# Kernel optimization log

Hardware: AMD Instinct MI355X
Metric: run time of the kernel (lower is better)

Reference implementation:

```python
import jax, jax.numpy as jnp
import numpy as np

HEADS = 16
DIM_HEAD = 64
WINDOW = 128
LOOK_BACKWARD = 1
LOOK_FORWARD = 0
THETA = 10000.0
PAD_VALUE = -1


def look_around(x, backward, forward, pad_value, axis):
    """Gather overlapping windows: concat shifted copies along the intra-window axis."""
    w = x.shape[axis]
    size = backward + forward + 1
    pads = [(0, 0)] * x.ndim
    pads[axis] = (backward, forward)
    p = jnp.pad(x, pads, constant_values=pad_value)
    segs = [jax.lax.slice_in_dim(p, s, s + w, axis=axis) for s in range(size)]
    return jnp.concatenate(segs, axis=axis + 1)


def rotate_half(t):
    t1, t2 = jnp.split(t, 2, axis=-1)
    return jnp.concatenate([-t2, t1], axis=-1)


def setup_inputs() -> dict:
    key = jax.random.key(0)
    k1, k2, k3 = jax.random.split(key, 3)
    dim = 1024
    x = jax.random.normal(k1, (4, 4096, dim), dtype=jnp.float32)
    W_qkv = jax.random.normal(k2, (dim, 3 * HEADS * DIM_HEAD), dtype=jnp.float32) * (dim ** -0.5)
    W_out = jax.random.normal(k3, (HEADS * DIM_HEAD, dim), dtype=jnp.float32) * ((HEADS * DIM_HEAD) ** -0.5)
    return {"x": x, "W_qkv": W_qkv, "W_out": W_out}


def reference(x, W_qkv, W_out):
    b, n, dim = x.shape
    h, dh, ws = HEADS, DIM_HEAD, WINDOW
    w = n // ws
    j = ws * (LOOK_BACKWARD + LOOK_FORWARD + 1)  # 256 keys per query window

    qkv = x @ W_qkv  # (b, n, 3*h*dh)
    q, k, v = jnp.split(qkv, 3, axis=-1)

    def to_bhwnd(t):
        return t.reshape(b, n, h, dh).transpose(0, 2, 1, 3).reshape(b, h, w, ws, dh)

    bq = to_bhwnd(q) * (dh ** -0.5)
    bk = look_around(to_bhwnd(k), LOOK_BACKWARD, LOOK_FORWARD, float(PAD_VALUE), axis=2)
    bv = look_around(to_bhwnd(v), LOOK_BACKWARD, LOOK_FORWARD, float(PAD_VALUE), axis=2)

    # rotary embeddings over the look-around key length; queries use last ws positions
    inv_freq = 1.0 / (THETA ** (jnp.arange(0, dh, 2, dtype=jnp.float32) / dh))
    t_pos = jnp.arange(j, dtype=jnp.float32)
    freqs = t_pos[:, None] * inv_freq[None, :]
    freqs = jnp.concatenate([freqs, freqs], axis=-1)  # (j, dh)
    q_freqs = freqs[-ws:]
    bq = bq * jnp.cos(q_freqs) + rotate_half(bq) * jnp.sin(q_freqs)
    bk = bk * jnp.cos(freqs) + rotate_half(bk) * jnp.sin(freqs)

    sim = jnp.einsum('bhwid,bhwjd->bhwij', bq, bk)  # (b,h,w,ws,j)

    seq = jnp.arange(n).reshape(w, ws)
    bq_t = seq[:, :, None]  # (w, ws, 1)
    bq_k = look_around(seq[None], LOOK_BACKWARD, LOOK_FORWARD, PAD_VALUE, axis=1)[0]  # (w, j)
    bq_k = bq_k[:, None, :]  # (w, 1, j)
    pad_mask = bq_k == PAD_VALUE
    # causal + exact window (look_backward * window_size)
    causal_mask = (bq_t < bq_k) | (bq_t > bq_k + ws * LOOK_BACKWARD)
    mask = causal_mask | pad_mask

    mask_value = -jnp.finfo(sim.dtype).max
    sim = jnp.where(mask, mask_value, sim)
    attn = jax.nn.softmax(sim, axis=-1)

    out = jnp.einsum('bhwij,bhwjd->bhwid', attn, bv)
    out = out.reshape(b, h, n, dh).transpose(0, 2, 1, 3).reshape(b, n, h * dh)
    return out @ W_out
```

## Files before the change

### kernel.cpp

```cpp
#include <hip/hip_runtime.h>
#include <stdint.h>


typedef __attribute__((ext_vector_type(8))) short bfrag;
typedef __attribute__((ext_vector_type(4))) float f4;

#define MFMA_BF16(a, b, c) __builtin_amdgcn_mfma_f32_16x16x32_bf16((a), (b), (c), 0, 0, 0)

static __device__ __forceinline__ short f2bf(float f) {
  unsigned u = __builtin_bit_cast(unsigned, f);
  u = (u + 0x7fffu + ((u >> 16) & 1u)) >> 16;
  return (short)u;
}
static __device__ __forceinline__ float bf2f(short s) {
  unsigned u = ((unsigned)(unsigned short)s) << 16;
  return __builtin_bit_cast(float, u);
}

typedef __attribute__((address_space(3))) unsigned lds_u;
typedef __attribute__((address_space(1))) unsigned gbl_u;

static __device__ __forceinline__ void gl_lds16(const void* g, const void* lds) {
  unsigned loff = (unsigned)__builtin_amdgcn_readfirstlane((int)(uintptr_t)lds);
  __builtin_amdgcn_global_load_lds((gbl_u*)(uintptr_t)g, (lds_u*)(uintptr_t)loff, 16, 0, 0);
}

__global__ __launch_bounds__(256) void convert_x(const float* __restrict__ x,
                                                 short* __restrict__ xb) {
  int idx = blockIdx.x * 256 + threadIdx.x;
  size_t base = (size_t)idx * 8;
  float4 a = *(const float4*)(x + base);
  float4 b = *(const float4*)(x + base + 4);
  bfrag o;
  o[0] = f2bf(a.x); o[1] = f2bf(a.y); o[2] = f2bf(a.z); o[3] = f2bf(a.w);
  o[4] = f2bf(b.x); o[5] = f2bf(b.y); o[6] = f2bf(b.z); o[7] = f2bf(b.w);
  *(bfrag*)(xb + base) = o;
}

__global__ __launch_bounds__(256) void transpose_w(
    const float* __restrict__ wqkv, const float* __restrict__ wout,
    short* __restrict__ wqkvT, short* __restrict__ woutT) {
  __shared__ short t[64][72];
  const int tid = threadIdx.x;
  const int kt = blockIdx.x, yt = blockIdx.y;
  const float* src; short* dst; int N, nt;
  if (yt < 48) { src = wqkv; dst = wqkvT; N = 3072; nt = yt; }
  else         { src = wout; dst = woutT; N = 1024; nt = yt - 48; }
  const int k0 = kt * 64, n0 = nt * 64;
#pragma unroll
  for (int i = 0; i < 4; ++i) {
    int r = i * 16 + (tid >> 4);
    int c = (tid & 15) * 4;
    float4 v = *(const float4*)(src + (size_t)(k0 + r) * N + n0 + c);
    t[c + 0][r] = f2bf(v.x);
    t[c + 1][r] = f2bf(v.y);
    t[c + 2][r] = f2bf(v.z);
    t[c + 3][r] = f2bf(v.w);
  }
  __syncthreads();
#pragma unroll
  for (int i = 0; i < 2; ++i) {
    int c = tid + i * 256;
    int n = c >> 3, k8 = (c & 7) * 8;
    *(bfrag*)(dst + (size_t)(n0 + n) * 1024 + k0 + k8) = *(const bfrag*)&t[n][k8];
  }
}

template <int MODE>
__global__ __launch_bounds__(256) void gemm_bt(
    const short* __restrict__ A, const short* __restrict__ Bt, float* __restrict__ C,
    short* __restrict__ oq, short* __restrict__ ok, short* __restrict__ ov) {
  __shared__ __align__(16) short Al[128 * 32];
  __shared__ __align__(16) short Bl[128 * 32];
  const int bx = blockIdx.x, by = blockIdx.y;
  const int tid = threadIdx.x, lane = tid & 63, wv = tid >> 6;
  const int wr = wv >> 1, wc = wv & 1;
  const int l15 = lane & 15, quad = lane >> 4;

  const short* Ab = A + (size_t)by * 128 * 1024;
  const short* Bb = Bt + (size_t)bx * 128 * 1024;

  const int c0 = wv * 128 + lane, c1 = c0 + 64;
  const int ra0 = c0 >> 2, oa0 = (c0 & 3) * 8;
  const int ra1 = c1 >> 2, oa1 = (c1 & 3) * 8;

  f4 acc[4][4];
#pragma unroll
  for (int i = 0; i < 4; ++i)
#pragma unroll
    for (int j = 0; j < 4; ++j) acc[i][j] = (f4)0.f;

  for (int kk = 0; kk < 1024; kk += 32) {
    gl_lds16(Ab + (size_t)ra0 * 1024 + kk + oa0, Al + c0 * 8);
    gl_lds16(Ab + (size_t)ra1 * 1024 + kk + oa1, Al + c1 * 8);
    gl_lds16(Bb + (size_t)ra0 * 1024 + kk + oa0, Bl + c0 * 8);
    gl_lds16(Bb + (size_t)ra1 * 1024 + kk + oa1, Bl + c1 * 8);
    __syncthreads();
    bfrag af[4], bfv[4];
#pragma unroll
    for (int t = 0; t < 4; ++t) af[t] = *(const bfrag*)&Al[(wr * 64 + t * 16 + l15) * 32 + quad * 8];
#pragma unroll
    for (int t = 0; t < 4; ++t) bfv[t] = *(const bfrag*)&Bl[(wc * 64 + t * 16 + l15) * 32 + quad * 8];
#pragma unroll
    for (int i = 0; i < 4; ++i)
#pragma unroll
      for (int j = 0; j < 4; ++j) acc[i][j] = MFMA_BF16(af[i], bfv[j], acc[i][j]);
    __syncthreads();
  }

  if (MODE == 0) {
    const int n64 = bx * 128 + wc * 64;
    const int part = n64 >> 10;
    const int head = (n64 & 1023) >> 6;
    short* o = (part == 0) ? oq : (part == 1) ? ok : ov;
    const float f0 = exp2f((float)l15 * -0.41524101186f);
    const float f1 = exp2f((float)(16 + l15) * -0.41524101186f);
#pragma unroll
    for (int i = 0; i < 4; ++i)
#pragma unroll
      for (int r = 0; r < 4; ++r) {
        const int m = by * 128 + wr * 64 + i * 16 + quad * 4 + r;
        const int b = m >> 12, p = m & 4095;
        short* row = o + ((size_t)(b * 16 + head) * 4096 + p) * 64;
        if (part == 2) {
#pragma unroll
          for (int j = 0; j < 4; ++j) row[j * 16 + l15] = f2bf(acc[i][j][r]);
        } else {
#pragma unroll
          for (int j = 0; j < 2; ++j) {
            float av = acc[i][j][r], bv2 = acc[i][j + 2][r];
            float sn, cs;
            __sincosf((float)p * (j ? f1 : f0), &sn, &cs);
            float ra = av * cs - bv2 * sn;
            float rb = bv2 * cs + av * sn;
            if (part == 0) { ra *= 0.125f; rb *= 0.125f; }
            row[j * 16 + l15] = f2bf(ra);
            row[32 + j * 16 + l15] = f2bf(rb);
          }
        }
      }
  } else {
#pragma unroll
    for (int i = 0; i < 4; ++i)
#pragma unroll
      for (int j = 0; j < 4; ++j)
#pragma unroll
        for (int r = 0; r < 4; ++r) {
          int m = by * 128 + wr * 64 + i * 16 + quad * 4 + r;
          int n = bx * 128 + wc * 64 + j * 16 + l15;
          C[(size_t)m * 1024 + n] = acc[i][j][r];
        }
  }
}

__global__ __launch_bounds__(256) void attn_kernel(
    const short* __restrict__ qb, const short* __restrict__ kb,
    const short* __restrict__ vb, short* __restrict__ ob) {
  constexpr int KST = 72, VST = 264, PST = 136;
  __shared__ __align__(16) short smem[18432 + 16896];
  short* Ks = smem;
  short* Pl = smem;
  short* Vt = smem + 18432;

  const int bid = blockIdx.x;
  const int w = bid & 31, bh = bid >> 5;
  const int tid = threadIdx.x, lane = tid & 63, wv = tid >> 6;
  const int l15 = lane & 15, quad = lane >> 4;
  const size_t kvbase = (size_t)bh * (4096 * 64);
  const int pk0 = w * 128 - 128;

  const int i0 = wv * 32;
  const short* qbase = qb + kvbase + (size_t)(w * 128) * 64;
  bfrag aq[2][2];
#pragma unroll
  for (int rt = 0; rt < 2; ++rt)
#pragma unroll
    for (int ks = 0; ks < 2; ++ks)
      aq[rt][ks] = *(const bfrag*)(qbase + (size_t)(i0 + rt * 16 + l15) * 64 + ks * 32 + quad * 8);

#pragma unroll
  for (int i = 0; i < 8; ++i) {
    int c = tid + i * 256;
    int row = c >> 3;
    int d0 = (c & 7) * 8;
    int pk = pk0 + row;
    if (pk < 0) pk = 0;
    const size_t src = kvbase + (size_t)pk * 64 + d0;
    bfrag kvv = *(const bfrag*)(kb + src);
    *(bfrag*)&Ks[row * KST + d0] = kvv;
    bfrag vvv = *(const bfrag*)(vb + src);
#pragma unroll
    for (int j = 0; j < 8; ++j) Vt[(d0 + j) * VST + row] = vvv[j];
  }
  __syncthreads();

  f4 sim[2][16];
#pragma unroll
  for (int rt = 0; rt < 2; ++rt)
#pragma unroll
    for (int ct = 0; ct < 16; ++ct) sim[rt][ct] = (f4)0.f;

#pragma unroll
  for (int ct = 0; ct < 16; ++ct) {
    bfrag bk0 = *(const bfrag*)&Ks[(ct * 16 + l15) * KST + quad * 8];
    bfrag bk1 = *(const bfrag*)&Ks[(ct * 16 + l15) * KST + 32 + quad * 8];
#pragma unroll
    for (int rt = 0; rt < 2; ++rt) {
      sim[rt][ct] = MFMA_BF16(aq[rt][0], bk0, sim[rt][ct]);
      sim[rt][ct] = MFMA_BF16(aq[rt][1], bk1, sim[rt][ct]);
    }
  }
  __syncthreads();

  float linv[2][4];
#pragma unroll
  for (int rt = 0; rt < 2; ++rt)
#pragma unroll
    for (int r = 0; r < 4; ++r) {
      const int iloc = i0 + rt * 16 + quad * 4 + r;
      float sum = 0.f;
#pragma unroll
      for (int ct = 0; ct < 16; ++ct) {
        int jj = ct * 16 + l15;
        bool valid = (jj >= iloc) && (jj <= iloc + 128) && ((w > 0) || (jj >= 128));
        float pv = valid ? __expf(sim[rt][ct][r]) : 0.f;
        sim[rt][ct][r] = pv;
        sum += pv;
      }
#pragma unroll
      for (int off = 1; off < 16; off <<= 1) sum += __shfl_xor(sum, off);
      linv[rt][r] = 1.f / sum;
    }

  f4 oacc[2][4];
#pragma unroll
  for (int rt = 0; rt < 2; ++rt)
#pragma unroll
    for (int ctd = 0; ctd < 4; ++ctd) oacc[rt][ctd] = (f4)0.f;

#pragma unroll
  for (int pass = 0; pass < 2; ++pass) {
#pragma unroll
    for (int rt = 0; rt < 2; ++rt)
#pragma unroll
      for (int ct = 0; ct < 8; ++ct) {
        int ctg = pass * 8 + ct;
#pragma unroll
        for (int r = 0; r < 4; ++r)
          Pl[(i0 + rt * 16 + quad * 4 + r) * PST + ct * 16 + l15] = f2bf(sim[rt][ctg][r]);
      }
#pragma unroll
    for (int ks = 0; ks < 4; ++ks) {
      bfrag ap[2];
#pragma unroll
      for (int rt = 0; rt < 2; ++rt)
        ap[rt] = *(const bfrag*)&Pl[(i0 + rt * 16 + l15) * PST + ks * 32 + quad * 8];
#pragma unroll
      for (int ctd = 0; ctd < 4; ++ctd) {
        bfrag bv = *(const bfrag*)&Vt[(ctd * 16 + l15) * VST + pass * 128 + ks * 32 + quad * 8];
#pragma unroll
        for (int rt = 0; rt < 2; ++rt) oacc[rt][ctd] = MFMA_BF16(ap[rt], bv, oacc[rt][ctd]);
      }
    }
  }

  const int b = bh >> 4, h = bh & 15;
  short* obase = ob + ((size_t)b * 4096 + w * 128) * 1024 + h * 64;
#pragma unroll
  for (int rt = 0; rt < 2; ++rt)
#pragma unroll
    for (int ctd = 0; ctd < 4; ++ctd)
#pragma unroll
      for (int r = 0; r < 4; ++r) {
        int i = i0 + rt * 16 + quad * 4 + r;
        int d = ctd * 16 + l15;
        obase[(size_t)i * 1024 + d] = f2bf(oacc[rt][ctd][r] * linv[rt][r]);
      }
}

extern "C" void kernel_launch(void* const* d_in, const int* in_sizes, int n_in,
                              void* d_out, int out_size, void* d_ws, size_t ws_size,
                              hipStream_t stream) {
  const float* x = (const float*)d_in[0];
  const float* wqkv = (const float*)d_in[1];
  const float* wout = (const float*)d_in[2];
  float* out = (float*)d_out;
  char* ws = (char*)d_ws;

  short* qb = (short*)(ws + 0);
  short* kb = (short*)(ws + 33554432);
  short* vb = (short*)(ws + 67108864);
  short* xb = (short*)(ws + 100663296);
  short* ab = xb;
  short* wqkvT = (short*)(ws + 134217728);
  short* woutT = (short*)(ws + 140509184);

  convert_x<<<8192, 256, 0, stream>>>(x, xb);
  transpose_w<<<dim3(16, 64), 256, 0, stream>>>(wqkv, wout, wqkvT, woutT);
  gemm_bt<0><<<dim3(24, 128), 256, 0, stream>>>(xb, wqkvT, nullptr, qb, kb, vb);
  attn_kernel<<<2048, 256, 0, stream>>>(qb, kb, vb, ab);
  gemm_bt<1><<<dim3(8, 128), 256, 0, stream>>>(ab, woutT, out, nullptr, nullptr, nullptr);
}
```

Before: 407.2 us.

## Replace GEMM with 256x256-tile double-buffered pipelined MFMA kernel

Replaces the 128x128-tile GEMM with a 512-thread, 256x256-tile kernel. It double-buffers A/B tiles in LDS through direct global-to-LDS loads and interleaves prefetch of the next k-slices with MFMA phases, using explicit vmcnt waits, barriers and s_setprio. Block IDs are remapped so neighbouring tiles are spread across XCD groups for better cache reuse. The aim is to hide global load latency and raise arithmetic intensity for both the QKV and output projections. In exchange it uses 128KB of LDS per block, which limits occupancy, and relies on hand-tuned wait counts.

```diff
diff --git a/kernel.cpp b/kernel.cpp
--- a/kernel.cpp
+++ b/kernel.cpp
@@ -66,60 +66,131 @@
   }
 }
 
-template <int MODE>
-__global__ __launch_bounds__(256) void gemm_bt(
+#define VM6 asm volatile("s_waitcnt vmcnt(6)" ::: "memory")
+#define VM4 asm volatile("s_waitcnt vmcnt(4)" ::: "memory")
+#define VM0 asm volatile("s_waitcnt vmcnt(0)" ::: "memory")
+#define VNOP ((void)0)
+
+#define ST_A(buf, ks, kk)                                                          \
+  do {                                                                             \
+    gl_lds16(aS0 + (ks) * 32 + (kk), ldsA + (buf) * 32768 + (ks) * 16384 + stA);   \
+    gl_lds16(aS1 + (ks) * 32 + (kk),                                               \
+             ldsA + (buf) * 32768 + (ks) * 16384 + 8192 + stA);                    \
+  } while (0)
+#define ST_B(buf, ks, kk)                                                          \
+  do {                                                                             \
+    gl_lds16(bS0 + (ks) * 32 + (kk), ldsB + (buf) * 32768 + (ks) * 16384 + stA);   \
+    gl_lds16(bS1 + (ks) * 32 + (kk),                                               \
+             ldsB + (buf) * 32768 + (ks) * 16384 + 8192 + stA);                    \
+  } while (0)
+
+#define MM4(mi, a)                                 \
+  acc[mi][0] = MFMA_BF16(a, b0, acc[mi][0]);       \
+  acc[mi][1] = MFMA_BF16(a, b1, acc[mi][1]);       \
+  acc[mi][2] = MFMA_BF16(a, b2, acc[mi][2]);       \
+  acc[mi][3] = MFMA_BF16(a, b3, acc[mi][3])
+
+#define PHASE(buf, ks, mh, STAGE, WAIT)                                            \
+  {                                                                                \
+    const char* pA_ = ldsA + (buf) * 32768 + (ks) * 16384 + (mh) * 4096 + aRd;     \
+    const char* pB_ = ldsB + (buf) * 32768 + (ks) * 16384 + bRd;                   \
+    bfrag a0 = *(const bfrag*)(pA_);                                               \
+    bfrag a1 = *(const bfrag*)(pA_ + 1024);                                        \
+    bfrag a2 = *(const bfrag*)(pA_ + 2048);                                        \
+    bfrag a3 = *(const bfrag*)(pA_ + 3072);                                        \
+    bfrag b0 = *(const bfrag*)(pB_);                                               \
+    bfrag b1 = *(const bfrag*)(pB_ + 1024);                                        \
+    bfrag b2 = *(const bfrag*)(pB_ + 2048);                                        \
+    bfrag b3 = *(const bfrag*)(pB_ + 3072);                                        \
+    STAGE;                                                                         \
+    WAIT;                                                                          \
+    __builtin_amdgcn_s_barrier();                                                  \
+    asm volatile("s_waitcnt lgkmcnt(0)" ::: "memory");                             \
+    __builtin_amdgcn_sched_barrier(0);                                             \
+    __builtin_amdgcn_s_setprio(1);                                                 \
+    MM4((mh) * 4 + 0, a0);                                                         \
+    MM4((mh) * 4 + 1, a1);                                                         \
+    MM4((mh) * 4 + 2, a2);                                                         \
+    MM4((mh) * 4 + 3, a3);                                                         \
+    __builtin_amdgcn_s_setprio(0);                                                 \
+    __builtin_amdgcn_s_barrier();                                                  \
+  }
+
+template <int MODE, int NBX>
+__global__ __launch_bounds__(512, 2) void gemm256(
     const short* __restrict__ A, const short* __restrict__ Bt, float* __restrict__ C,
     short* __restrict__ oq, short* __restrict__ ok, short* __restrict__ ov) {
-  __shared__ __align__(16) short Al[128 * 32];
-  __shared__ __align__(16) short Bl[128 * 32];
-  const int bx = blockIdx.x, by = blockIdx.y;
+  __shared__ __align__(1024) char lds[131072];
+  char* const ldsA = lds;
+  char* const ldsB = lds + 65536;
+
   const int tid = threadIdx.x, lane = tid & 63, wv = tid >> 6;
-  const int wr = wv >> 1, wc = wv & 1;
+  const int wr = wv >> 2, wc = wv & 3;
   const int l15 = lane & 15, quad = lane >> 4;
 
-  const short* Ab = A + (size_t)by * 128 * 1024;
-  const short* Bb = Bt + (size_t)bx * 128 * 1024;
-
-  const int c0 = wv * 128 + lane, c1 = c0 + 64;
-  const int ra0 = c0 >> 2, oa0 = (c0 & 3) * 8;
-  const int ra1 = c1 >> 2, oa1 = (c1 & 3) * 8;
-
-  f4 acc[4][4];
-#pragma unroll
-  for (int i = 0; i < 4; ++i)
+  const int nwg = NBX * 64;
+  const int bid = (int)blockIdx.x;
+  const int wgid = (bid & 7) * (nwg >> 3) + (bid >> 3);
+  const int bx = wgid % NBX, by = wgid / NBX;
+
+  const short* Ab = A + (size_t)by * 256 * 1024;
+  const short* Bb = Bt + (size_t)bx * 256 * 1024;
+
+  const int srow = lane & 15, scg = lane >> 4;
+  const short* aS0 = Ab + (size_t)(wv * 16 + srow) * 1024 + scg * 8;
+  const short* aS1 = Ab + (size_t)((8 + wv) * 16 + srow) * 1024 + scg * 8;
+  const short* bS0 = Bb + (size_t)(wv * 16 + srow) * 1024 + scg * 8;
+  const short* bS1 = Bb + (size_t)((8 + wv) * 16 + srow) * 1024 + scg * 8;
+  const int stA = wv * 1024;
+
+  const int rdoff = lane * 16;
+  const int aRd = wr * 8192 + rdoff;
+  const int bRd = wc * 4096 + rdoff;
+
+  f4 acc[8][4];
+#pragma unroll
+  for (int i = 0; i < 8; ++i)
 #pragma unroll
     for (int j = 0; j < 4; ++j) acc[i][j] = (f4)0.f;
 
-  for (int kk = 0; kk < 1024; kk += 32) {
-    gl_lds16(Ab + (size_t)ra0 * 1024 + kk + oa0, Al + c0 * 8);
-    gl_lds16(Ab + (size_t)ra1 * 1024 + kk + oa1, Al + c1 * 8);
-    gl_lds16(Bb + (size_t)ra0 * 1024 + kk + oa0, Bl + c0 * 8);
-    gl_lds16(Bb + (size_t)ra1 * 1024 + kk + oa1, Bl + c1 * 8);
-    __syncthreads();
-    bfrag af[4], bfv[4];
-#pragma unroll
-    for (int t = 0; t < 4; ++t) af[t] = *(const bfrag*)&Al[(wr * 64 + t * 16 + l15) * 32 + quad * 8];
-#pragma unroll
-    for (int t = 0; t < 4; ++t) bfv[t] = *(const bfrag*)&Bl[(wc * 64 + t * 16 + l15) * 32 + quad * 8];
-#pragma unroll
-    for (int i = 0; i < 4; ++i)
-#pragma unroll
-      for (int j = 0; j < 4; ++j) acc[i][j] = MFMA_BF16(af[i], bfv[j], acc[i][j]);
-    __syncthreads();
-  }
-
-  if (MODE == 0) {
-    const int n64 = bx * 128 + wc * 64;
+  ST_A(0, 0, 0); ST_B(0, 0, 0); ST_A(0, 1, 0); ST_B(0, 1, 0); ST_A(1, 0, 64);
+  VM6;
+  __builtin_amdgcn_s_barrier();
+
+#pragma unroll 1
+  for (int t = 0; t < 14; t += 2) {
+    const int kk1 = t * 64 + 64, kk2 = t * 64 + 128, kk3 = t * 64 + 192;
+    PHASE(0, 0, 0, ST_B(1, 0, kk1), VNOP);
+    PHASE(0, 0, 1, ST_A(1, 1, kk1), VM6);
+    PHASE(0, 1, 0, ST_B(1, 1, kk1), VNOP);
+    PHASE(0, 1, 1, ST_A(0, 0, kk2), VM6);
+    PHASE(1, 0, 0, ST_B(0, 0, kk2), VNOP);
+    PHASE(1, 0, 1, ST_A(0, 1, kk2), VM6);
+    PHASE(1, 1, 0, ST_B(0, 1, kk2), VNOP);
+    PHASE(1, 1, 1, ST_A(1, 0, kk3), VM6);
+  }
+
+  PHASE(0, 0, 0, ST_B(1, 0, 960), VNOP);
+  PHASE(0, 0, 1, ST_A(1, 1, 960), VM6);
+  PHASE(0, 1, 0, ST_B(1, 1, 960), VNOP);
+  PHASE(0, 1, 1, VNOP, VM4);
+  PHASE(1, 0, 0, VNOP, VNOP);
+  PHASE(1, 0, 1, VNOP, VM0);
+  PHASE(1, 1, 0, VNOP, VNOP);
+  PHASE(1, 1, 1, VNOP, VNOP);
+
+  if constexpr (MODE == 0) {
+    const int n64 = bx * 256 + wc * 64;
     const int part = n64 >> 10;
     const int head = (n64 & 1023) >> 6;
     short* o = (part == 0) ? oq : (part == 1) ? ok : ov;
     const float f0 = exp2f((float)l15 * -0.41524101186f);
     const float f1 = exp2f((float)(16 + l15) * -0.41524101186f);
 #pragma unroll
-    for (int i = 0; i < 4; ++i)
+    for (int i = 0; i < 8; ++i)
 #pragma unroll
       for (int r = 0; r < 4; ++r) {
-        const int m = by * 128 + wr * 64 + i * 16 + quad * 4 + r;
+        const int m = by * 256 + wr * 128 + i * 16 + quad * 4 + r;
         const int b = m >> 12, p = m & 4095;
         short* row = o + ((size_t)(b * 16 + head) * 4096 + p) * 64;
         if (part == 2) {
@@ -141,13 +212,13 @@
       }
   } else {
 #pragma unroll
-    for (int i = 0; i < 4; ++i)
+    for (int i = 0; i < 8; ++i)
 #pragma unroll
       for (int j = 0; j < 4; ++j)
 #pragma unroll
         for (int r = 0; r < 4; ++r) {
-          int m = by * 128 + wr * 64 + i * 16 + quad * 4 + r;
-          int n = bx * 128 + wc * 64 + j * 16 + l15;
+          int m = by * 256 + wr * 128 + i * 16 + quad * 4 + r;
+          int n = bx * 256 + wc * 64 + j * 16 + l15;
           C[(size_t)m * 1024 + n] = acc[i][j][r];
         }
   }
@@ -297,7 +368,7 @@
 
   convert_x<<<8192, 256, 0, stream>>>(x, xb);
   transpose_w<<<dim3(16, 64), 256, 0, stream>>>(wqkv, wout, wqkvT, woutT);
-  gemm_bt<0><<<dim3(24, 128), 256, 0, stream>>>(xb, wqkvT, nullptr, qb, kb, vb);
+  gemm256<0, 12><<<768, 512, 0, stream>>>(xb, wqkvT, nullptr, qb, kb, vb);
   attn_kernel<<<2048, 256, 0, stream>>>(qb, kb, vb, ab);
-  gemm_bt<1><<<dim3(8, 128), 256, 0, stream>>>(ab, woutT, out, nullptr, nullptr, nullptr);
-}
+  gemm256<1, 4><<<256, 512, 0, stream>>>(ab, woutT, out, nullptr, nullptr, nullptr);
+}
```

Measured after the change: 361.5 us. 11.2% less time.
